# Kernel tuning notes

Measured on AMD Instinct MI355X. Metric: run time of the kernel, lower is better.

The kernel has to match this reference:

```python
import jax, jax.numpy as jnp
import numpy as np

N = 8192
F_IN = 256
F_OUT = 256


def setup_inputs() -> dict:
    key = jax.random.key(0)
    k1, k2, k3 = jax.random.split(key, 3)
    H = jax.random.normal(k1, (N, F_IN), dtype=jnp.float32)
    A_tilde = jax.random.uniform(k2, (N, N), dtype=jnp.float32)  # positive -> valid degrees
    # xavier_uniform for W: limit = sqrt(6/(fan_in+fan_out))
    limit = np.sqrt(6.0 / (F_IN + F_OUT)).astype(np.float32)
    W = jax.random.uniform(k3, (F_IN, F_OUT), dtype=jnp.float32, minval=-limit, maxval=limit)
    return {"H": H, "A_tilde": A_tilde, "W": W}


def reference(H, A_tilde, W):
    # H(l+1) = relu(D^-1/2 A D^-1/2 H W)
    # Diagonal matmuls expressed as row/col rescaling (same math, O(N^2)).
    d_inv_sqrt = jnp.sum(A_tilde, axis=1) ** -0.5          # [N]
    A_norm = d_inv_sqrt[:, None] * A_tilde * d_inv_sqrt[None, :]  # [N,N]
    H_next = (A_norm @ H) @ W                              # [N,F_out]
    return jax.nn.relu(H_next)
```

## Files before the change

### kernel.cpp

```cpp
#include <hip/hip_runtime.h>
#include <hip/hip_bf16.h>

#define N_ROWS 8192
#define F_DIM  256

typedef __bf16 bf16x8_t __attribute__((ext_vector_type(8)));
typedef float  f32x4_t  __attribute__((ext_vector_type(4)));

static __device__ __forceinline__ unsigned short f2bf(float x) {
    union { __hip_bfloat16 h; unsigned short u; } c;
    c.h = __float2bfloat16(x);
    return c.u;
}
static __device__ __forceinline__ unsigned pk2(float lo, float hi) {
    return (unsigned)f2bf(lo) | ((unsigned)f2bf(hi) << 16);
}

__global__ __launch_bounds__(256) void wconv_kernel(const float* __restrict__ W,
                                                    unsigned short* __restrict__ Ws) {
    const int kb = blockIdx.x;
    const int t  = threadIdx.x;
    __shared__ float wt[32][257];
    const int r = t >> 3, g = t & 7;
    const float* src = W + (kb * 32 + r) * F_DIM + g * 32;
#pragma unroll
    for (int i = 0; i < 8; ++i) {
        float4 v = *(const float4*)(src + i * 4);
        wt[r][g * 32 + i * 4 + 0] = v.x;
        wt[r][g * 32 + i * 4 + 1] = v.y;
        wt[r][g * 32 + i * 4 + 2] = v.z;
        wt[r][g * 32 + i * 4 + 3] = v.w;
    }
    __syncthreads();
    unsigned o[16];
#pragma unroll
    for (int k = 0; k < 32; k += 2) o[k >> 1] = pk2(wt[k][t], wt[k + 1][t]);
    uint4* dst = (uint4*)(Ws + kb * 8192 + t * 32);
#pragma unroll
    for (int i = 0; i < 4; ++i) dst[i] = make_uint4(o[4*i], o[4*i+1], o[4*i+2], o[4*i+3]);
}

__global__ __launch_bounds__(1024) void prep_kernel(const float* __restrict__ A,
                                                    const float* __restrict__ H,
                                                    float* __restrict__ dvec,
                                                    unsigned short* __restrict__ Xs) {
    const int kb = blockIdx.x;
    const int t  = threadIdx.x;
    __shared__ float psum[32][33];
    __shared__ float dl[32];
    __shared__ float ht[32][257];

    const int r = t >> 5, g = t & 31;
    const float* arow = A + (size_t)(kb * 32 + r) * N_ROWS;
    float s0 = 0.f, s1 = 0.f, s2 = 0.f, s3 = 0.f;
#pragma unroll 8
    for (int i = 0; i < 64; ++i) {
        float4 v = *(const float4*)(arow + (i * 32 + g) * 4);
        s0 += v.x; s1 += v.y; s2 += v.z; s3 += v.w;
    }
    psum[r][g] = (s0 + s1) + (s2 + s3);
    __syncthreads();
    if (t < 32) {
        float s = 0.f;
#pragma unroll
        for (int i = 0; i < 32; ++i) s += psum[t][i];
        float d = 1.0f / sqrtf(s);
        dl[t] = d;
        dvec[kb * 32 + t] = d;
    }
    __syncthreads();
    {
        const int hr = t >> 5, hg = t & 31;
        const float* hsrc = H + (size_t)(kb * 32 + hr) * F_DIM + hg * 8;
        float4 v0 = ((const float4*)hsrc)[0];
        float4 v1 = ((const float4*)hsrc)[1];
        const float d = dl[hr];
        ht[hr][hg * 8 + 0] = v0.x * d;
        ht[hr][hg * 8 + 1] = v0.y * d;
        ht[hr][hg * 8 + 2] = v0.z * d;
        ht[hr][hg * 8 + 3] = v0.w * d;
        ht[hr][hg * 8 + 4] = v1.x * d;
        ht[hr][hg * 8 + 5] = v1.y * d;
        ht[hr][hg * 8 + 6] = v1.z * d;
        ht[hr][hg * 8 + 7] = v1.w * d;
    }
    __syncthreads();
    const int n = t >> 2, q = t & 3;
    unsigned o[4];
#pragma unroll
    for (int i = 0; i < 4; ++i) {
        int k = q * 8 + i * 2;
        o[i] = pk2(ht[k][n], ht[k + 1][n]);
    }
    *(uint4*)(Xs + kb * 8192 + n * 32 + q * 8) = make_uint4(o[0], o[1], o[2], o[3]);
}

template <int KITERS, int ASTRIDE, bool DSCALE, bool RELU>
__global__ __launch_bounds__(512) void gemm_kernel(const float* __restrict__ Amat,
                                                   const unsigned short* __restrict__ Bs,
                                                   const float* __restrict__ dvec,
                                                   float* __restrict__ out) {
    const int t   = threadIdx.x;
    const int blk = blockIdx.x;
    const int w = t >> 6, l = t & 63;
    const int m = l & 15, q = l >> 4;

    __shared__ __align__(16) unsigned short Al[2][1024];

    const int ar = t >> 4, ac = (t & 15) * 2;
    const float* aptr = Amat + (size_t)(blk * 32 + ar) * ASTRIDE + ac;
    const int wr_idx = (ac >> 3) * 256 + (ar >> 4) * 128 + (ar & 15) * 8 + (ac & 7);

    const unsigned short* bptr = Bs + (w * 32 + m) * 32 + q * 8;

    f32x4_t acc[2][2] = {};

    float2 a_cur[2]; uint4 b_cur[2][2];
#pragma unroll
    for (int s = 0; s < 2; ++s) {
        a_cur[s]    = *(const float2*)(aptr + s * 32);
        b_cur[s][0] = *(const uint4*)(bptr + s * 8192);
        b_cur[s][1] = *(const uint4*)(bptr + s * 8192 + 512);
    }

    for (int i = 0; i < KITERS; ++i) {
        float2 a_nxt[2]; uint4 b_nxt[2][2];
        if (i + 1 < KITERS) {
            const float* ap = aptr + (i + 1) * 64;
            const unsigned short* bp = bptr + (size_t)(i + 1) * 16384;
#pragma unroll
            for (int s = 0; s < 2; ++s) {
                a_nxt[s]    = *(const float2*)(ap + s * 32);
                b_nxt[s][0] = *(const uint4*)(bp + s * 8192);
                b_nxt[s][1] = *(const uint4*)(bp + s * 8192 + 512);
            }
        }
        const unsigned aw0 = pk2(a_cur[0].x, a_cur[0].y);
        const unsigned aw1 = pk2(a_cur[1].x, a_cur[1].y);
        __syncthreads();
        *(unsigned*)&Al[0][wr_idx] = aw0;
        *(unsigned*)&Al[1][wr_idx] = aw1;
        __syncthreads();
#pragma unroll
        for (int s = 0; s < 2; ++s) {
            bf16x8_t af0 = *(const bf16x8_t*)&Al[s][q * 256 + m * 8];
            bf16x8_t af1 = *(const bf16x8_t*)&Al[s][q * 256 + 128 + m * 8];
            bf16x8_t bf0 = __builtin_bit_cast(bf16x8_t, b_cur[s][0]);
            bf16x8_t bf1 = __builtin_bit_cast(bf16x8_t, b_cur[s][1]);
            acc[0][0] = __builtin_amdgcn_mfma_f32_16x16x32_bf16(af0, bf0, acc[0][0], 0, 0, 0);
            acc[0][1] = __builtin_amdgcn_mfma_f32_16x16x32_bf16(af0, bf1, acc[0][1], 0, 0, 0);
            acc[1][0] = __builtin_amdgcn_mfma_f32_16x16x32_bf16(af1, bf0, acc[1][0], 0, 0, 0);
            acc[1][1] = __builtin_amdgcn_mfma_f32_16x16x32_bf16(af1, bf1, acc[1][1], 0, 0, 0);
        }
#pragma unroll
        for (int s = 0; s < 2; ++s) {
            a_cur[s]    = a_nxt[s];
            b_cur[s][0] = b_nxt[s][0];
            b_cur[s][1] = b_nxt[s][1];
        }
    }

    const int gcol0 = w * 32 + m;
#pragma unroll
    for (int mt = 0; mt < 2; ++mt) {
#pragma unroll
        for (int r = 0; r < 4; ++r) {
            const int grow = blk * 32 + mt * 16 + q * 4 + r;
            float ds = 1.0f;
            if (DSCALE) ds = dvec[grow];
#pragma unroll
            for (int nt = 0; nt < 2; ++nt) {
                float v = acc[mt][nt][r] * ds;
                if (RELU) v = fmaxf(v, 0.f);
                out[(size_t)grow * F_DIM + gcol0 + nt * 16] = v;
            }
        }
    }
}

extern "C" void kernel_launch(void* const* d_in, const int* in_sizes, int n_in,
                              void* d_out, int out_size, void* d_ws, size_t ws_size,
                              hipStream_t stream) {
    (void)in_sizes; (void)n_in; (void)out_size; (void)ws_size;
    const float* H = (const float*)d_in[0];
    const float* A = (const float*)d_in[1];
    const float* W = (const float*)d_in[2];
    float* out = (float*)d_out;

    char* ws = (char*)d_ws;
    float*          dvec = (float*)ws;
    unsigned short* Xs   = (unsigned short*)(ws + (32 << 10));
    unsigned short* Wsz  = (unsigned short*)(ws + (32 << 10) + (4 << 20));
    float*          Y    = (float*)(ws + (32 << 10) + (4 << 20) + (128 << 10));

    wconv_kernel<<<dim3(8),   dim3(256),  0, stream>>>(W, Wsz);
    prep_kernel <<<dim3(256), dim3(1024), 0, stream>>>(A, H, dvec, Xs);
    gemm_kernel<128, 8192, true,  false><<<dim3(256), dim3(512), 0, stream>>>(A, Xs, dvec, Y);
    gemm_kernel<4,   256,  false, true ><<<dim3(256), dim3(512), 0, stream>>>(Y, Wsz, nullptr, out);
}
```

Baseline: 464.7 us.

## Reassociate to A·(HW), pre-convert A to bf16, split-K big GEMM

The pass is reassociated to compute X2 = (D^-1/2 H) W first, then A·X2 as the big GEMM. While summing rows, the prep kernel also writes A as bf16, and the big GEMM loads that bf16 A directly into LDS via global_load_lds with 64x256 tiles. Work is split four ways along K, followed by a separate reduce kernel that applies d scaling and ReLU. This adds a 128MB bf16 copy of A plus write/read traffic and a partial-sum buffer. In exchange the large GEMM reads half the bytes and uses larger tiles with more parallelism.

```diff
diff --git a/kernel.cpp b/kernel.cpp
--- a/kernel.cpp
+++ b/kernel.cpp
@@ -3,6 +3,7 @@
 
 #define N_ROWS 8192
 #define F_DIM  256
+#define KSPLIT 4
 
 typedef __bf16 bf16x8_t __attribute__((ext_vector_type(8)));
 typedef float  f32x4_t  __attribute__((ext_vector_type(4)));
@@ -14,6 +15,11 @@
 }
 static __device__ __forceinline__ unsigned pk2(float lo, float hi) {
     return (unsigned)f2bf(lo) | ((unsigned)f2bf(hi) << 16);
+}
+
+static __device__ __forceinline__ void gload16(const unsigned short* g, unsigned short* s) {
+    __builtin_amdgcn_global_load_lds((const __attribute__((address_space(1))) void*)g,
+                                     (__attribute__((address_space(3))) void*)s, 16, 0, 0);
 }
 
 __global__ __launch_bounds__(256) void wconv_kernel(const float* __restrict__ W,
@@ -40,23 +46,28 @@
     for (int i = 0; i < 4; ++i) dst[i] = make_uint4(o[4*i], o[4*i+1], o[4*i+2], o[4*i+3]);
 }
 
-__global__ __launch_bounds__(1024) void prep_kernel(const float* __restrict__ A,
-                                                    const float* __restrict__ H,
-                                                    float* __restrict__ dvec,
-                                                    unsigned short* __restrict__ Xs) {
+__global__ __launch_bounds__(1024) void sumconv_kernel(const float* __restrict__ A,
+                                                       const float* __restrict__ H,
+                                                       float* __restrict__ dvec,
+                                                       unsigned short* __restrict__ Abf,
+                                                       unsigned short* __restrict__ Xrm) {
     const int kb = blockIdx.x;
     const int t  = threadIdx.x;
     __shared__ float psum[32][33];
     __shared__ float dl[32];
-    __shared__ float ht[32][257];
 
     const int r = t >> 5, g = t & 31;
-    const float* arow = A + (size_t)(kb * 32 + r) * N_ROWS;
+    const int row = kb * 32 + r;
+    const float* arow = A + (size_t)row * N_ROWS;
+    unsigned short* aout = Abf + (size_t)row * N_ROWS;
     float s0 = 0.f, s1 = 0.f, s2 = 0.f, s3 = 0.f;
 #pragma unroll 8
     for (int i = 0; i < 64; ++i) {
-        float4 v = *(const float4*)(arow + (i * 32 + g) * 4);
+        const int e = (i * 32 + g) * 4;
+        float4 v = *(const float4*)(arow + e);
         s0 += v.x; s1 += v.y; s2 += v.z; s3 += v.w;
+        uint2 p = make_uint2(pk2(v.x, v.y), pk2(v.z, v.w));
+        *(uint2*)(aout + e) = p;
     }
     psum[r][g] = (s0 + s1) + (s2 + s3);
     __syncthreads();
@@ -71,111 +82,148 @@
     __syncthreads();
     {
         const int hr = t >> 5, hg = t & 31;
-        const float* hsrc = H + (size_t)(kb * 32 + hr) * F_DIM + hg * 8;
+        const int hrow = kb * 32 + hr;
+        const float* hsrc = H + (size_t)hrow * F_DIM + hg * 8;
         float4 v0 = ((const float4*)hsrc)[0];
         float4 v1 = ((const float4*)hsrc)[1];
         const float d = dl[hr];
-        ht[hr][hg * 8 + 0] = v0.x * d;
-        ht[hr][hg * 8 + 1] = v0.y * d;
-        ht[hr][hg * 8 + 2] = v0.z * d;
-        ht[hr][hg * 8 + 3] = v0.w * d;
-        ht[hr][hg * 8 + 4] = v1.x * d;
-        ht[hr][hg * 8 + 5] = v1.y * d;
-        ht[hr][hg * 8 + 6] = v1.z * d;
-        ht[hr][hg * 8 + 7] = v1.w * d;
-    }
-    __syncthreads();
-    const int n = t >> 2, q = t & 3;
-    unsigned o[4];
-#pragma unroll
-    for (int i = 0; i < 4; ++i) {
-        int k = q * 8 + i * 2;
-        o[i] = pk2(ht[k][n], ht[k + 1][n]);
-    }
-    *(uint4*)(Xs + kb * 8192 + n * 32 + q * 8) = make_uint4(o[0], o[1], o[2], o[3]);
-}
-
-template <int KITERS, int ASTRIDE, bool DSCALE, bool RELU>
-__global__ __launch_bounds__(512) void gemm_kernel(const float* __restrict__ Amat,
-                                                   const unsigned short* __restrict__ Bs,
-                                                   const float* __restrict__ dvec,
-                                                   float* __restrict__ out) {
-    const int t   = threadIdx.x;
-    const int blk = blockIdx.x;
+        uint4 o = make_uint4(pk2(v0.x * d, v0.y * d), pk2(v0.z * d, v0.w * d),
+                             pk2(v1.x * d, v1.y * d), pk2(v1.z * d, v1.w * d));
+        *(uint4*)(Xrm + (size_t)hrow * F_DIM + hg * 8) = o;
+    }
+}
+
+__global__ __launch_bounds__(256) void x2gemm_kernel(const unsigned short* __restrict__ Xrm,
+                                                     const unsigned short* __restrict__ Ws,
+                                                     unsigned short* __restrict__ X2s) {
+    const int t = threadIdx.x;
     const int w = t >> 6, l = t & 63;
-    const int m = l & 15, q = l >> 4;
-
-    __shared__ __align__(16) unsigned short Al[2][1024];
-
-    const int ar = t >> 4, ac = (t & 15) * 2;
-    const float* aptr = Amat + (size_t)(blk * 32 + ar) * ASTRIDE + ac;
-    const int wr_idx = (ac >> 3) * 256 + (ar >> 4) * 128 + (ar & 15) * 8 + (ac & 7);
-
-    const unsigned short* bptr = Bs + (w * 32 + m) * 32 + q * 8;
-
-    f32x4_t acc[2][2] = {};
-
-    float2 a_cur[2]; uint4 b_cur[2][2];
-#pragma unroll
-    for (int s = 0; s < 2; ++s) {
-        a_cur[s]    = *(const float2*)(aptr + s * 32);
-        b_cur[s][0] = *(const uint4*)(bptr + s * 8192);
-        b_cur[s][1] = *(const uint4*)(bptr + s * 8192 + 512);
-    }
-
+    const int m16 = l & 15, q = l >> 4, q8 = q * 8;
+    const int rbase = blockIdx.x * 64 + w * 16;
+
+    f32x4_t acc[16] = {};
+    const unsigned short* ap = Xrm + (size_t)(rbase + m16) * F_DIM + q8;
+#pragma unroll
+    for (int kb = 0; kb < 8; ++kb) {
+        bf16x8_t af = __builtin_bit_cast(bf16x8_t, *(const uint4*)(ap + kb * 32));
+        const unsigned short* bp = Ws + kb * 8192 + m16 * 32 + q8;
+#pragma unroll
+        for (int nt = 0; nt < 16; ++nt) {
+            bf16x8_t bf = __builtin_bit_cast(bf16x8_t, *(const uint4*)(bp + nt * 512));
+            acc[nt] = __builtin_amdgcn_mfma_f32_16x16x32_bf16(af, bf, acc[nt], 0, 0, 0);
+        }
+    }
+    const int kr0 = rbase + q * 4;
+    unsigned short* op = X2s + (kr0 >> 5) * 8192 + m16 * 32 + (kr0 & 31);
+#pragma unroll
+    for (int nt = 0; nt < 16; ++nt) {
+        uint2 o = make_uint2(pk2(acc[nt][0], acc[nt][1]), pk2(acc[nt][2], acc[nt][3]));
+        *(uint2*)(op + nt * 512) = o;
+    }
+}
+
+__global__ __launch_bounds__(256, 2) void biggemm_kernel(const unsigned short* __restrict__ Abf,
+                                                         const unsigned short* __restrict__ X2s,
+                                                         float* __restrict__ Ypart) {
+    const int t = threadIdx.x;
+    const int w = t >> 6, l = t & 63;
+    const int m16 = l & 15, q = l >> 4, q8 = q * 8;
+    const int bid = blockIdx.x;
+    const int ks = bid & 3, mi = bid >> 2;
+    const int kbase = ks * 2048;
+
+    __shared__ __align__(16) unsigned short lds[2][4096];
+
+    const unsigned short* ag[2];
+    int aslot[2];
+#pragma unroll
+    for (int j = 0; j < 2; ++j) {
+        const int idx = w * 2 + j, ft = idx >> 1, s = idx & 1;
+        ag[j] = Abf + (size_t)(mi * 64 + ft * 16 + m16) * N_ROWS + kbase + s * 32 + q8;
+        aslot[j] = idx * 512;
+    }
+    const unsigned short* bptr = X2s + (kbase >> 5) * 8192 + (w * 64 + m16) * 32 + q8;
+
+    f32x4_t acc[4][4] = {};
+
+#pragma unroll
+    for (int j = 0; j < 2; ++j) gload16(ag[j], &lds[0][aslot[j]]);
+    uint4 bcur[2][4];
+#pragma unroll
+    for (int s = 0; s < 2; ++s)
+#pragma unroll
+        for (int nt = 0; nt < 4; ++nt)
+            bcur[s][nt] = *(const uint4*)(bptr + s * 8192 + nt * 512);
+
+    const int KITERS = 2048 / 64;
     for (int i = 0; i < KITERS; ++i) {
-        float2 a_nxt[2]; uint4 b_nxt[2][2];
+        __syncthreads();
+        const int cb = i & 1;
+        uint4 bnxt[2][4];
         if (i + 1 < KITERS) {
-            const float* ap = aptr + (i + 1) * 64;
-            const unsigned short* bp = bptr + (size_t)(i + 1) * 16384;
-#pragma unroll
-            for (int s = 0; s < 2; ++s) {
-                a_nxt[s]    = *(const float2*)(ap + s * 32);
-                b_nxt[s][0] = *(const uint4*)(bp + s * 8192);
-                b_nxt[s][1] = *(const uint4*)(bp + s * 8192 + 512);
+#pragma unroll
+            for (int j = 0; j < 2; ++j)
+                gload16(ag[j] + (i + 1) * 64, &lds[cb ^ 1][aslot[j]]);
+            const unsigned short* bp = bptr + (i + 1) * 16384;
+#pragma unroll
+            for (int s = 0; s < 2; ++s)
+#pragma unroll
+                for (int nt = 0; nt < 4; ++nt)
+                    bnxt[s][nt] = *(const uint4*)(bp + s * 8192 + nt * 512);
+        }
+#pragma unroll
+        for (int s = 0; s < 2; ++s) {
+            bf16x8_t af[4];
+#pragma unroll
+            for (int mt = 0; mt < 4; ++mt)
+                af[mt] = *(const bf16x8_t*)&lds[cb][(mt * 2 + s) * 512 + l * 8];
+#pragma unroll
+            for (int mt = 0; mt < 4; ++mt)
+#pragma unroll
+                for (int nt = 0; nt < 4; ++nt)
+                    acc[mt][nt] = __builtin_amdgcn_mfma_f32_16x16x32_bf16(
+                        af[mt], __builtin_bit_cast(bf16x8_t, bcur[s][nt]), acc[mt][nt], 0, 0, 0);
+        }
+#pragma unroll
+        for (int s = 0; s < 2; ++s)
+#pragma unroll
+            for (int nt = 0; nt < 4; ++nt)
+                bcur[s][nt] = bnxt[s][nt];
+    }
+
+    float* Y = Ypart + (size_t)ks * (N_ROWS * F_DIM);
+#pragma unroll
+    for (int mt = 0; mt < 4; ++mt) {
+#pragma unroll
+        for (int r = 0; r < 4; ++r) {
+            const int row = mi * 64 + mt * 16 + q * 4 + r;
+#pragma unroll
+            for (int nt = 0; nt < 4; ++nt) {
+                const int col = w * 64 + nt * 16 + m16;
+                Y[(size_t)row * F_DIM + col] = acc[mt][nt][r];
             }
         }
-        const unsigned aw0 = pk2(a_cur[0].x, a_cur[0].y);
-        const unsigned aw1 = pk2(a_cur[1].x, a_cur[1].y);
-        __syncthreads();
-        *(unsigned*)&Al[0][wr_idx] = aw0;
-        *(unsigned*)&Al[1][wr_idx] = aw1;
-        __syncthreads();
-#pragma unroll
-        for (int s = 0; s < 2; ++s) {
-            bf16x8_t af0 = *(const bf16x8_t*)&Al[s][q * 256 + m * 8];
-            bf16x8_t af1 = *(const bf16x8_t*)&Al[s][q * 256 + 128 + m * 8];
-            bf16x8_t bf0 = __builtin_bit_cast(bf16x8_t, b_cur[s][0]);
-            bf16x8_t bf1 = __builtin_bit_cast(bf16x8_t, b_cur[s][1]);
-            acc[0][0] = __builtin_amdgcn_mfma_f32_16x16x32_bf16(af0, bf0, acc[0][0], 0, 0, 0);
-            acc[0][1] = __builtin_amdgcn_mfma_f32_16x16x32_bf16(af0, bf1, acc[0][1], 0, 0, 0);
-            acc[1][0] = __builtin_amdgcn_mfma_f32_16x16x32_bf16(af1, bf0, acc[1][0], 0, 0, 0);
-            acc[1][1] = __builtin_amdgcn_mfma_f32_16x16x32_bf16(af1, bf1, acc[1][1], 0, 0, 0);
-        }
-#pragma unroll
-        for (int s = 0; s < 2; ++s) {
-            a_cur[s]    = a_nxt[s];
-            b_cur[s][0] = b_nxt[s][0];
-            b_cur[s][1] = b_nxt[s][1];
-        }
-    }
-
-    const int gcol0 = w * 32 + m;
-#pragma unroll
-    for (int mt = 0; mt < 2; ++mt) {
-#pragma unroll
-        for (int r = 0; r < 4; ++r) {
-            const int grow = blk * 32 + mt * 16 + q * 4 + r;
-            float ds = 1.0f;
-            if (DSCALE) ds = dvec[grow];
-#pragma unroll
-            for (int nt = 0; nt < 2; ++nt) {
-                float v = acc[mt][nt][r] * ds;
-                if (RELU) v = fmaxf(v, 0.f);
-                out[(size_t)grow * F_DIM + gcol0 + nt * 16] = v;
-            }
-        }
-    }
+    }
+}
+
+__global__ __launch_bounds__(256) void reduce_kernel(const float* __restrict__ Ypart,
+                                                     const float* __restrict__ dvec,
+                                                     float* __restrict__ out) {
+    const int idx = blockIdx.x * 256 + threadIdx.x;
+    const int row = idx >> 6;
+    const float d = dvec[row];
+    const size_t YS = (size_t)N_ROWS * F_DIM / 4;
+    const float4* yp = (const float4*)Ypart;
+    float4 a = yp[idx];
+    float4 b = yp[idx + YS];
+    float4 c = yp[idx + 2 * YS];
+    float4 e = yp[idx + 3 * YS];
+    float4 o;
+    o.x = fmaxf(d * (a.x + b.x + c.x + e.x), 0.f);
+    o.y = fmaxf(d * (a.y + b.y + c.y + e.y), 0.f);
+    o.z = fmaxf(d * (a.z + b.z + c.z + e.z), 0.f);
+    o.w = fmaxf(d * (a.w + b.w + c.w + e.w), 0.f);
+    ((float4*)out)[idx] = o;
 }
 
 extern "C" void kernel_launch(void* const* d_in, const int* in_sizes, int n_in,
@@ -188,13 +236,17 @@
     float* out = (float*)d_out;
 
     char* ws = (char*)d_ws;
-    float*          dvec = (float*)ws;
-    unsigned short* Xs   = (unsigned short*)(ws + (32 << 10));
-    unsigned short* Wsz  = (unsigned short*)(ws + (32 << 10) + (4 << 20));
-    float*          Y    = (float*)(ws + (32 << 10) + (4 << 20) + (128 << 10));
-
-    wconv_kernel<<<dim3(8),   dim3(256),  0, stream>>>(W, Wsz);
-    prep_kernel <<<dim3(256), dim3(1024), 0, stream>>>(A, H, dvec, Xs);
-    gemm_kernel<128, 8192, true,  false><<<dim3(256), dim3(512), 0, stream>>>(A, Xs, dvec, Y);
-    gemm_kernel<4,   256,  false, true ><<<dim3(256), dim3(512), 0, stream>>>(Y, Wsz, nullptr, out);
-}
+    size_t off = 0;
+    float*          dvec = (float*)(ws + off);           off += (32 << 10);
+    unsigned short* Xrm  = (unsigned short*)(ws + off);  off += (4 << 20);
+    unsigned short* Wsz  = (unsigned short*)(ws + off);  off += (128 << 10);
+    unsigned short* X2s  = (unsigned short*)(ws + off);  off += (4 << 20);
+    float*          Yp   = (float*)(ws + off);           off += (size_t)KSPLIT * N_ROWS * F_DIM * 4;
+    unsigned short* Abf  = (unsigned short*)(ws + off);  off += (size_t)N_ROWS * N_ROWS * 2;
+
+    wconv_kernel  <<<dim3(8),    dim3(256),  0, stream>>>(W, Wsz);
+    sumconv_kernel<<<dim3(256),  dim3(1024), 0, stream>>>(A, H, dvec, Abf, Xrm);
+    x2gemm_kernel <<<dim3(128),  dim3(256),  0, stream>>>(Xrm, Wsz, X2s);
+    biggemm_kernel<<<dim3(512),  dim3(256),  0, stream>>>(Abf, X2s, Yp);
+    reduce_kernel <<<dim3(2048), dim3(256),  0, stream>>>(Yp, dvec, out);
+}
```

After: 522.3 us. 1.12x slower.
